# Kernel optimization log

Measured on AMD Instinct MI355X. Metric: run time of the kernel, lower is better.

The kernel has to match this reference:

```python
import jax, jax.numpy as jnp
import numpy as np

B, N, K, C, CE, H = 2, 2048, 48, 128, 128, 128
IN = 2 * C + CE  # 384
AGG_SCALE = 30.0
LN_EPS = 1e-5


def setup_inputs() -> dict:
    key = jax.random.key(0)
    ks = jax.random.split(key, 12)
    inp = {
        "node_h": jax.random.normal(ks[0], (B, N, C), jnp.float32),
        "edge_h": jax.random.normal(ks[1], (B, N, K, CE), jnp.float32),
        "edge_index": jax.random.randint(ks[2], (B, N, K), 0, N, jnp.int64),
        # message MLP: Linear(IN,H) GELU Linear(H,H) GELU Linear(H,C)
        "W1": jax.random.normal(ks[3], (IN, H), jnp.float32) / np.sqrt(IN),
        "b1": jnp.zeros((H,), jnp.float32),
        "W2": jax.random.normal(ks[4], (H, H), jnp.float32) / np.sqrt(H),
        "b2": jnp.zeros((H,), jnp.float32),
        "W3": jax.random.normal(ks[5], (H, C), jnp.float32) / np.sqrt(H),
        "b3": jnp.zeros((C,), jnp.float32),
        "Wu": jax.random.normal(ks[6], (C, C), jnp.float32) / np.sqrt(C),
        "bu": jnp.zeros((C,), jnp.float32),
        "ln_g": jnp.ones((C,), jnp.float32),
        "ln_b": jnp.zeros((C,), jnp.float32),
    }
    return inp


def _layer_norm(x, g, b):
    mu = jnp.mean(x, axis=-1, keepdims=True)
    var = jnp.var(x, axis=-1, keepdims=True)
    return (x - mu) * jax.lax.rsqrt(var + LN_EPS) * g + b


def _gelu(x):
    return jax.nn.gelu(x, approximate=False)  # torch nn.GELU default (erf)


def reference(node_h, edge_h, edge_index, W1, b1, W2, b2, W3, b3, Wu, bu, ln_g, ln_b):
    b, n, k = edge_index.shape
    c = node_h.shape[-1]
    # gather neighbor node features: (B,N,K,C)
    node_j = jnp.take_along_axis(
        node_h, edge_index.reshape(b, n * k)[..., None], axis=1
    ).reshape(b, n, k, c)
    node_i = jnp.broadcast_to(node_h[:, :, None, :], (b, n, k, c))
    edge_packed = jnp.concatenate([node_i, node_j, edge_h], axis=-1)  # (B,N,K,IN)
    # message MLP
    h = _gelu(edge_packed @ W1 + b1)
    h = _gelu(h @ W2 + b2)
    messages = (h @ W3 + b3).sum(axis=-2) / AGG_SCALE  # (B,N,C)
    # dropout is identity in eval mode
    updated_nodes = _layer_norm(node_h + messages, ln_g, ln_b)
    node_updates = updated_nodes @ Wu + bu
    out = _layer_norm(node_h + node_updates, ln_g, ln_b)
    return out
```

## Files before the change

### kernel.cpp

```cpp
#include <hip/hip_runtime.h>
#include <hip/hip_bf16.h>
#include <math.h>

#define Bn   2
#define Nn   2048
#define Kn   48
#define Cn   128
#define G2   16

typedef short bf16x8 __attribute__((ext_vector_type(8)));
typedef float f32x4  __attribute__((ext_vector_type(4)));

#if __has_builtin(__builtin_amdgcn_cvt_pk_bf16_f32)
#define HAS_PK 1
#endif

__device__ __forceinline__ short f2bf(float f) {
  union { float f; unsigned u; } v; v.f = f;
  unsigned r = v.u + 0x7fffu + ((v.u >> 16) & 1u);
  return (short)(r >> 16);
}

__device__ __forceinline__ unsigned pk2(float a, float b) {
#ifdef HAS_PK
  auto p = __builtin_amdgcn_cvt_pk_bf16_f32(a, b);
  return __builtin_bit_cast(unsigned, p);
#else
  return (unsigned)(unsigned short)f2bf(a) | ((unsigned)(unsigned short)f2bf(b) << 16);
#endif
}

__device__ __forceinline__ float gelu_f(float x) {
  float z = x * (-2.3021991f - 0.10294200f * x * x);
  float e = __builtin_amdgcn_exp2f(z);
  return x * __builtin_amdgcn_rcpf(1.0f + e);
}

__global__ void pack_weights(const float* __restrict__ W1,
                             const float* __restrict__ W2,
                             const float* __restrict__ W3,
                             const float* __restrict__ Wu,
                             short* __restrict__ ws) {
  int tid = blockIdx.x * blockDim.x + threadIdx.x;
  if (tid >= 192 * 64) return;
  int lane = tid & 63;
  int tile = tid >> 6;
  const float* W; short* dst;
  if (tile < 32)       { W = W1;         dst = ws; }
  else if (tile < 96)  { W = W1 + 16384; dst = ws + 16384; tile -= 32; }
  else if (tile < 128) { W = W2;         dst = ws + 49152; tile -= 96; }
  else if (tile < 160) { W = W3;         dst = ws + 65536; tile -= 128; }
  else                 { W = Wu;         dst = ws + 81920; tile -= 160; }
  int kt = tile >> 3, nt = tile & 7;
  int n  = nt * 16 + (lane & 15);
  int k0 = kt * 32 + (lane >> 4) * 8;
  union { short s[8]; bf16x8 v; } u8;
#pragma unroll
  for (int j = 0; j < 8; j++) u8.s[j] = f2bf(W[(k0 + j) * 128 + n]);
  *reinterpret_cast<bf16x8*>(dst + (tile << 9) + lane * 8) = u8.v;
}

__global__ __launch_bounds__(512, 8)
void node_update_kernel(const float* __restrict__ node_h,
                        const float* __restrict__ edge_h,
                        const int*   __restrict__ edge_index,
                        const short* __restrict__ wpack,
                        const float* __restrict__ b1,
                        const float* __restrict__ b2,
                        float* __restrict__ hs_out) {
  __shared__ __align__(16) char smem[25472];
  short* Xs    = (short*)smem;
  short* H1s   = (short*)smem;
  short* nhb   = (short*)(smem + 24576);
  int*   idx_s = (int*)  (smem + 25088);

  const int tid  = threadIdx.x;
  const int n0   = blockIdx.x * 2;
  const int bb   = n0 >> 11;
  const int lane = tid & 63;
  const int wave = tid >> 6;
  const int lr   = lane & 15;
  const int lq   = lane >> 4;

  const short* W1i = wpack;
  const short* W1e = wpack + 16384;
  const short* W2p = wpack + 49152;

  if (tid < 256) {
    nhb[tid] = f2bf(node_h[(size_t)n0 * Cn + tid]);
  } else if (tid < 352) {
    idx_s[tid - 256] = edge_index[n0 * Kn + (tid - 256)];
  }
  __syncthreads();

  const int gw = tid & 15;
  const int gr = tid >> 4;
#pragma unroll
  for (int k = 0; k < 3; k++) {
    int r = gr + k * 32;
    const float* src = node_h + (size_t)(bb * Nn + idx_s[r]) * Cn + gw * 8;
    float4 v0 = *reinterpret_cast<const float4*>(src);
    float4 v1 = *reinterpret_cast<const float4*>(src + 4);
    uint4 p;
    p.x = pk2(v0.x, v0.y); p.y = pk2(v0.z, v0.w);
    p.z = pk2(v1.x, v1.y); p.w = pk2(v1.z, v1.w);
    *reinterpret_cast<uint4*>(&Xs[r * 128 + ((gw ^ (r & 7)) << 3)]) = p;
  }
  __syncthreads();

  f32x4 accY[2] = {};
#pragma unroll
  for (int kt = 0; kt < 4; kt++) {
    bf16x8 avA = {}, avB = {};
    if (lr == 0) {
      avA = *reinterpret_cast<const bf16x8*>(&nhb[kt * 32 + lq * 8]);
      avB = *reinterpret_cast<const bf16x8*>(&nhb[128 + kt * 32 + lq * 8]);
    }
    bf16x8 bv = *reinterpret_cast<const bf16x8*>(W1i + ((kt * 8 + wave) << 9) + lane * 8);
    accY[0] = __builtin_amdgcn_mfma_f32_16x16x32_bf16(avA, bv, accY[0], 0, 0, 0);
    accY[1] = __builtin_amdgcn_mfma_f32_16x16x32_bf16(avB, bv, accY[1], 0, 0, 0);
  }

  f32x4 acc[6] = {};
#pragma unroll
  for (int kt = 0; kt < 4; kt++) {
    bf16x8 bf = *reinterpret_cast<const bf16x8*>(W1e + ((kt * 8 + wave) << 9) + lane * 8);
    int sw = (((kt * 4 + lq) ^ (lr & 7)) << 3);
#pragma unroll
    for (int m = 0; m < 6; m++) {
      bf16x8 a = *reinterpret_cast<const bf16x8*>(&Xs[(m * 16 + lr) * 128 + sw]);
      acc[m] = __builtin_amdgcn_mfma_f32_16x16x32_bf16(a, bf, acc[m], 0, 0, 0);
    }
  }
  __syncthreads();

#pragma unroll
  for (int k = 0; k < 3; k++) {
    int r = gr + k * 32;
    const float* src = edge_h + ((size_t)n0 * Kn + r) * Cn + gw * 8;
    float4 v0 = *reinterpret_cast<const float4*>(src);
    float4 v1 = *reinterpret_cast<const float4*>(src + 4);
    uint4 p;
    p.x = pk2(v0.x, v0.y); p.y = pk2(v0.z, v0.w);
    p.z = pk2(v1.x, v1.y); p.w = pk2(v1.z, v1.w);
    *reinterpret_cast<uint4*>(&Xs[r * 128 + ((gw ^ (r & 7)) << 3)]) = p;
  }
  __syncthreads();

#pragma unroll
  for (int kt = 4; kt < 8; kt++) {
    bf16x8 bf = *reinterpret_cast<const bf16x8*>(W1e + ((kt * 8 + wave) << 9) + lane * 8);
    int sw = ((((kt - 4) * 4 + lq) ^ (lr & 7)) << 3);
#pragma unroll
    for (int m = 0; m < 6; m++) {
      bf16x8 a = *reinterpret_cast<const bf16x8*>(&Xs[(m * 16 + lr) * 128 + sw]);
      acc[m] = __builtin_amdgcn_mfma_f32_16x16x32_bf16(a, bf, acc[m], 0, 0, 0);
    }
  }
  __syncthreads();

  {
    int col = wave * 16 + lr;
    float yiA = __shfl(accY[0][0], lr) + b1[col];
    float yiB = __shfl(accY[1][0], lr) + b1[col];
    int g = col >> 3, cl = col & 7;
#pragma unroll
    for (int mt = 0; mt < 6; mt++) {
      float yi = (mt < 3) ? yiA : yiB;
      int r0 = mt * 16 + lq * 4;
      float g0 = gelu_f(acc[mt][0] + yi);
      float g1 = gelu_f(acc[mt][1] + yi);
      float g2 = gelu_f(acc[mt][2] + yi);
      float g3 = gelu_f(acc[mt][3] + yi);
      unsigned p01 = pk2(g0, g1), p23 = pk2(g2, g3);
      H1s[(r0 + 0) * 128 + ((g ^ ((r0 + 0) & 7)) << 3) + cl] = (short)(p01 & 0xffff);
      H1s[(r0 + 1) * 128 + ((g ^ ((r0 + 1) & 7)) << 3) + cl] = (short)(p01 >> 16);
      H1s[(r0 + 2) * 128 + ((g ^ ((r0 + 2) & 7)) << 3) + cl] = (short)(p23 & 0xffff);
      H1s[(r0 + 3) * 128 + ((g ^ ((r0 + 3) & 7)) << 3) + cl] = (short)(p23 >> 16);
    }
  }
  __syncthreads();

  f32x4 acc2[6] = {};
#pragma unroll
  for (int kt = 0; kt < 4; kt++) {
    bf16x8 bf = *reinterpret_cast<const bf16x8*>(W2p + ((kt * 8 + wave) << 9) + lane * 8);
    int sw = (((kt * 4 + lq) ^ (lr & 7)) << 3);
#pragma unroll
    for (int m = 0; m < 6; m++) {
      bf16x8 a = *reinterpret_cast<const bf16x8*>(&H1s[(m * 16 + lr) * 128 + sw]);
      acc2[m] = __builtin_amdgcn_mfma_f32_16x16x32_bf16(a, bf, acc2[m], 0, 0, 0);
    }
  }
  {
    int col = wave * 16 + lr;
    float bias = b2[col];
    float sA = 0.f, sB = 0.f;
#pragma unroll
    for (int mt = 0; mt < 3; mt++)
#pragma unroll
      for (int r = 0; r < 4; r++) {
        sA += gelu_f(acc2[mt][r] + bias);
        sB += gelu_f(acc2[mt + 3][r] + bias);
      }
    sA += __shfl_xor(sA, 16);
    sA += __shfl_xor(sA, 32);
    sB += __shfl_xor(sB, 16);
    sB += __shfl_xor(sB, 32);
    if (lq == 0) {
      hs_out[(size_t)n0 * Cn + col]       = sA;
      hs_out[(size_t)(n0 + 1) * Cn + col] = sB;
    }
  }
}

__global__ __launch_bounds__(256, 4)
void tail_kernel(const float* __restrict__ node_h,
                 const short* __restrict__ wpack,
                 const float* __restrict__ b3,
                 const float* __restrict__ bu,
                 const float* __restrict__ ln_g,
                 const float* __restrict__ ln_b,
                 float* __restrict__ out) {
  __shared__ __align__(16) char sm2[24832];
  short* hsB = (short*)sm2;
  float* nhr = (float*)(sm2 + 4096);
  float* xs  = (float*)(sm2 + 12288);
  short* usB = (short*)(sm2 + 20736);

  const int tid  = threadIdx.x;
  const int lane = tid & 63;
  const int wave = tid >> 6;
  const int lr   = lane & 15;
  const int lq   = lane >> 4;
  const int n0   = blockIdx.x * G2;

  const short* W3p = wpack + 65536;
  const short* Wup = wpack + 81920;

  {
    int row = tid >> 4, seg = tid & 15;
    const float* p = node_h + (size_t)(n0 + row) * Cn + seg * 8;
    float4 a0 = *reinterpret_cast<const float4*>(p);
    float4 a1 = *reinterpret_cast<const float4*>(p + 4);
    *reinterpret_cast<float4*>(&nhr[row * 128 + seg * 8])     = a0;
    *reinterpret_cast<float4*>(&nhr[row * 128 + seg * 8 + 4]) = a1;
    const float* q = out + (size_t)(n0 + row) * Cn + seg * 8;
    float4 c0 = *reinterpret_cast<const float4*>(q);
    float4 c1 = *reinterpret_cast<const float4*>(q + 4);
    uint4 pk;
    pk.x = pk2(c0.x, c0.y); pk.y = pk2(c0.z, c0.w);
    pk.z = pk2(c1.x, c1.y); pk.w = pk2(c1.z, c1.w);
    *reinterpret_cast<uint4*>(&hsB[row * 128 + ((seg ^ (row & 7)) << 3)]) = pk;
  }
  __syncthreads();

  f32x4 am[2] = {};
#pragma unroll
  for (int kt = 0; kt < 4; kt++) {
    bf16x8 av = *reinterpret_cast<const bf16x8*>(&hsB[lr * 128 + (((kt * 4 + lq) ^ (lr & 7)) << 3)]);
    bf16x8 bv0 = *reinterpret_cast<const bf16x8*>(W3p + ((kt * 8 + wave * 2 + 0) << 9) + lane * 8);
    bf16x8 bv1 = *reinterpret_cast<const bf16x8*>(W3p + ((kt * 8 + wave * 2 + 1) << 9) + lane * 8);
    am[0] = __builtin_amdgcn_mfma_f32_16x16x32_bf16(av, bv0, am[0], 0, 0, 0);
    am[1] = __builtin_amdgcn_mfma_f32_16x16x32_bf16(av, bv1, am[1], 0, 0, 0);
  }
#pragma unroll
  for (int j = 0; j < 2; j++) {
    int col = (wave * 2 + j) * 16 + lr;
    float bb = 48.0f * b3[col];
#pragma unroll
    for (int r = 0; r < 4; r++) {
      int row = lq * 4 + r;
      xs[row * 132 + col] = nhr[row * 128 + col] + (am[j][r] + bb) * (1.0f / 30.0f);
    }
  }
  __syncthreads();

  const float lg1 = ln_g[lane],      lb1v = ln_b[lane];
  const float lg2 = ln_g[lane + 64], lb2v = ln_b[lane + 64];
#pragma unroll
  for (int s = 0; s < 4; s++) {
    int row = wave * 4 + s;
    float v1 = xs[row * 132 + lane];
    float v2 = xs[row * 132 + lane + 64];
    float s1 = v1 + v2, s2 = v1 * v1 + v2 * v2;
#pragma unroll
    for (int off = 32; off >= 1; off >>= 1) {
      s1 += __shfl_xor(s1, off);
      s2 += __shfl_xor(s2, off);
    }
    float mu = s1 * (1.f / 128.f);
    float var = s2 * (1.f / 128.f) - mu * mu;
    float rstd = rsqrtf(var + 1e-5f);
    unsigned u12 = pk2((v1 - mu) * rstd * lg1 + lb1v,
                       (v2 - mu) * rstd * lg2 + lb2v);
    int sw = (row & 7);
    usB[row * 128 + (((lane >> 3) ^ sw) << 3) + (lane & 7)]       = (short)(u12 & 0xffff);
    usB[row * 128 + ((((lane >> 3) + 8) ^ sw) << 3) + (lane & 7)] = (short)(u12 >> 16);
  }
  __syncthreads();

  f32x4 au[2] = {};
#pragma unroll
  for (int kt = 0; kt < 4; kt++) {
    bf16x8 av = *reinterpret_cast<const bf16x8*>(&usB[lr * 128 + (((kt * 4 + lq) ^ (lr & 7)) << 3)]);
    bf16x8 bv0 = *reinterpret_cast<const bf16x8*>(Wup + ((kt * 8 + wave * 2 + 0) << 9) + lane * 8);
    bf16x8 bv1 = *reinterpret_cast<const bf16x8*>(Wup + ((kt * 8 + wave * 2 + 1) << 9) + lane * 8);
    au[0] = __builtin_amdgcn_mfma_f32_16x16x32_bf16(av, bv0, au[0], 0, 0, 0);
    au[1] = __builtin_amdgcn_mfma_f32_16x16x32_bf16(av, bv1, au[1], 0, 0, 0);
  }
  __syncthreads();
#pragma unroll
  for (int j = 0; j < 2; j++) {
    int col = (wave * 2 + j) * 16 + lr;
    float bb = bu[col];
#pragma unroll
    for (int r = 0; r < 4; r++) {
      int row = lq * 4 + r;
      xs[row * 132 + col] = nhr[row * 128 + col] + au[j][r] + bb;
    }
  }
  __syncthreads();

#pragma unroll
  for (int s = 0; s < 4; s++) {
    int row = wave * 4 + s;
    float v1 = xs[row * 132 + lane];
    float v2 = xs[row * 132 + lane + 64];
    float s1 = v1 + v2, s2 = v1 * v1 + v2 * v2;
#pragma unroll
    for (int off = 32; off >= 1; off >>= 1) {
      s1 += __shfl_xor(s1, off);
      s2 += __shfl_xor(s2, off);
    }
    float mu = s1 * (1.f / 128.f);
    float var = s2 * (1.f / 128.f) - mu * mu;
    float rstd = rsqrtf(var + 1e-5f);
    out[(size_t)(n0 + row) * Cn + lane]      = (v1 - mu) * rstd * lg1 + lb1v;
    out[(size_t)(n0 + row) * Cn + lane + 64] = (v2 - mu) * rstd * lg2 + lb2v;
  }
}

extern "C" void kernel_launch(void* const* d_in, const int* in_sizes, int n_in,
                              void* d_out, int out_size, void* d_ws, size_t ws_size,
                              hipStream_t stream) {
  const float* node_h     = (const float*)d_in[0];
  const float* edge_h     = (const float*)d_in[1];
  const int*   edge_index = (const int*)  d_in[2];
  const float* W1 = (const float*)d_in[3];
  const float* b1 = (const float*)d_in[4];
  const float* W2 = (const float*)d_in[5];
  const float* b2 = (const float*)d_in[6];
  const float* W3 = (const float*)d_in[7];
  const float* b3 = (const float*)d_in[8];
  const float* Wu = (const float*)d_in[9];
  const float* bu = (const float*)d_in[10];
  const float* ln_g = (const float*)d_in[11];
  const float* ln_b = (const float*)d_in[12];
  float* out   = (float*)d_out;
  short* wpack = (short*)d_ws;

  pack_weights<<<48, 256, 0, stream>>>(W1, W2, W3, Wu, wpack);
  node_update_kernel<<<(Bn * Nn) / 2, 512, 0, stream>>>(
      node_h, edge_h, edge_index, wpack, b1, b2, out);
  tail_kernel<<<(Bn * Nn) / G2, 256, 0, stream>>>(
      node_h, wpack, b3, bu, ln_g, ln_b, out);
}
```

Baseline: 209.0 us.

## Prefetch gathered rows, edge features and weights into registers to overlap loads

The node_update kernel now issues the global loads for neighbour rows, weight fragments, biases and edge_h into registers early. Those loads run while earlier MFMA work (the node_i projection and the first half of the layer-1 GEMM) executes, and the bf16 pack and LDS store happen later. This is meant to hide global memory latency behind compute instead of stalling at each gather-then-sync step. The extra live registers force the launch-bounds occupancy hint down from 8 to 6, which may reduce latency hiding across waves.

```diff
diff --git a/kernel.cpp b/kernel.cpp
--- a/kernel.cpp
+++ b/kernel.cpp
@@ -60,7 +60,7 @@
   *reinterpret_cast<bf16x8*>(dst + (tile << 9) + lane * 8) = u8.v;
 }
 
-__global__ __launch_bounds__(512, 8)
+__global__ __launch_bounds__(512, 6)
 void node_update_kernel(const float* __restrict__ node_h,
                         const float* __restrict__ edge_h,
                         const int*   __restrict__ edge_index,
@@ -86,6 +86,14 @@
   const short* W1e = wpack + 16384;
   const short* W2p = wpack + 49152;
 
+  bf16x8 w1i[4];
+#pragma unroll
+  for (int kt = 0; kt < 4; kt++)
+    w1i[kt] = *reinterpret_cast<const bf16x8*>(W1i + ((kt * 8 + wave) << 9) + lane * 8);
+  const int colw = wave * 16 + lr;
+  const float b1v = b1[colw];
+  const float b2v = b2[colw];
+
   if (tid < 256) {
     nhb[tid] = f2bf(node_h[(size_t)n0 * Cn + tid]);
   } else if (tid < 352) {
@@ -95,18 +103,15 @@
 
   const int gw = tid & 15;
   const int gr = tid >> 4;
+
+  float4 na[3], nb[3];
 #pragma unroll
   for (int k = 0; k < 3; k++) {
     int r = gr + k * 32;
     const float* src = node_h + (size_t)(bb * Nn + idx_s[r]) * Cn + gw * 8;
-    float4 v0 = *reinterpret_cast<const float4*>(src);
-    float4 v1 = *reinterpret_cast<const float4*>(src + 4);
-    uint4 p;
-    p.x = pk2(v0.x, v0.y); p.y = pk2(v0.z, v0.w);
-    p.z = pk2(v1.x, v1.y); p.w = pk2(v1.z, v1.w);
-    *reinterpret_cast<uint4*>(&Xs[r * 128 + ((gw ^ (r & 7)) << 3)]) = p;
-  }
-  __syncthreads();
+    na[k] = *reinterpret_cast<const float4*>(src);
+    nb[k] = *reinterpret_cast<const float4*>(src + 4);
+  }
 
   f32x4 accY[2] = {};
 #pragma unroll
@@ -116,15 +121,60 @@
       avA = *reinterpret_cast<const bf16x8*>(&nhb[kt * 32 + lq * 8]);
       avB = *reinterpret_cast<const bf16x8*>(&nhb[128 + kt * 32 + lq * 8]);
     }
-    bf16x8 bv = *reinterpret_cast<const bf16x8*>(W1i + ((kt * 8 + wave) << 9) + lane * 8);
-    accY[0] = __builtin_amdgcn_mfma_f32_16x16x32_bf16(avA, bv, accY[0], 0, 0, 0);
-    accY[1] = __builtin_amdgcn_mfma_f32_16x16x32_bf16(avB, bv, accY[1], 0, 0, 0);
+    accY[0] = __builtin_amdgcn_mfma_f32_16x16x32_bf16(avA, w1i[kt], accY[0], 0, 0, 0);
+    accY[1] = __builtin_amdgcn_mfma_f32_16x16x32_bf16(avB, w1i[kt], accY[1], 0, 0, 0);
+  }
+  const float yiA = __shfl(accY[0][0], lr) + b1v;
+  const float yiB = __shfl(accY[1][0], lr) + b1v;
+
+#pragma unroll
+  for (int k = 0; k < 3; k++) {
+    int r = gr + k * 32;
+    uint4 p;
+    p.x = pk2(na[k].x, na[k].y); p.y = pk2(na[k].z, na[k].w);
+    p.z = pk2(nb[k].x, nb[k].y); p.w = pk2(nb[k].z, nb[k].w);
+    *reinterpret_cast<uint4*>(&Xs[r * 128 + ((gw ^ (r & 7)) << 3)]) = p;
+  }
+  __syncthreads();
+
+  bf16x8 w1a[4];
+#pragma unroll
+  for (int kt = 0; kt < 4; kt++)
+    w1a[kt] = *reinterpret_cast<const bf16x8*>(W1e + ((kt * 8 + wave) << 9) + lane * 8);
+  float4 ea[3], eb[3];
+#pragma unroll
+  for (int k = 0; k < 3; k++) {
+    int r = gr + k * 32;
+    const float* src = edge_h + ((size_t)n0 * Kn + r) * Cn + gw * 8;
+    ea[k] = *reinterpret_cast<const float4*>(src);
+    eb[k] = *reinterpret_cast<const float4*>(src + 4);
   }
 
   f32x4 acc[6] = {};
 #pragma unroll
   for (int kt = 0; kt < 4; kt++) {
-    bf16x8 bf = *reinterpret_cast<const bf16x8*>(W1e + ((kt * 8 + wave) << 9) + lane * 8);
+    int sw = (((kt * 4 + lq) ^ (lr & 7)) << 3);
+#pragma unroll
+    for (int m = 0; m < 6; m++) {
+      bf16x8 a = *reinterpret_cast<const bf16x8*>(&Xs[(m * 16 + lr) * 128 + sw]);
+      acc[m] = __builtin_amdgcn_mfma_f32_16x16x32_bf16(a, w1a[kt], acc[m], 0, 0, 0);
+    }
+  }
+  __syncthreads();
+
+#pragma unroll
+  for (int k = 0; k < 3; k++) {
+    int r = gr + k * 32;
+    uint4 p;
+    p.x = pk2(ea[k].x, ea[k].y); p.y = pk2(ea[k].z, ea[k].w);
+    p.z = pk2(eb[k].x, eb[k].y); p.w = pk2(eb[k].z, eb[k].w);
+    *reinterpret_cast<uint4*>(&Xs[r * 128 + ((gw ^ (r & 7)) << 3)]) = p;
+  }
+  __syncthreads();
+
+#pragma unroll
+  for (int kt = 0; kt < 4; kt++) {
+    bf16x8 bf = *reinterpret_cast<const bf16x8*>(W1e + (((kt + 4) * 8 + wave) << 9) + lane * 8);
     int sw = (((kt * 4 + lq) ^ (lr & 7)) << 3);
 #pragma unroll
     for (int m = 0; m < 6; m++) {
@@ -134,36 +184,8 @@
   }
   __syncthreads();
 
-#pragma unroll
-  for (int k = 0; k < 3; k++) {
-    int r = gr + k * 32;
-    const float* src = edge_h + ((size_t)n0 * Kn + r) * Cn + gw * 8;
-    float4 v0 = *reinterpret_cast<const float4*>(src);
-    float4 v1 = *reinterpret_cast<const float4*>(src + 4);
-    uint4 p;
-    p.x = pk2(v0.x, v0.y); p.y = pk2(v0.z, v0.w);
-    p.z = pk2(v1.x, v1.y); p.w = pk2(v1.z, v1.w);
-    *reinterpret_cast<uint4*>(&Xs[r * 128 + ((gw ^ (r & 7)) << 3)]) = p;
-  }
-  __syncthreads();
-
-#pragma unroll
-  for (int kt = 4; kt < 8; kt++) {
-    bf16x8 bf = *reinterpret_cast<const bf16x8*>(W1e + ((kt * 8 + wave) << 9) + lane * 8);
-    int sw = ((((kt - 4) * 4 + lq) ^ (lr & 7)) << 3);
-#pragma unroll
-    for (int m = 0; m < 6; m++) {
-      bf16x8 a = *reinterpret_cast<const bf16x8*>(&Xs[(m * 16 + lr) * 128 + sw]);
-      acc[m] = __builtin_amdgcn_mfma_f32_16x16x32_bf16(a, bf, acc[m], 0, 0, 0);
-    }
-  }
-  __syncthreads();
-
   {
-    int col = wave * 16 + lr;
-    float yiA = __shfl(accY[0][0], lr) + b1[col];
-    float yiB = __shfl(accY[1][0], lr) + b1[col];
-    int g = col >> 3, cl = col & 7;
+    int g = colw >> 3, cl = colw & 7;
 #pragma unroll
     for (int mt = 0; mt < 6; mt++) {
       float yi = (mt < 3) ? yiA : yiB;
@@ -193,23 +215,21 @@
     }
   }
   {
-    int col = wave * 16 + lr;
-    float bias = b2[col];
     float sA = 0.f, sB = 0.f;
 #pragma unroll
     for (int mt = 0; mt < 3; mt++)
 #pragma unroll
       for (int r = 0; r < 4; r++) {
-        sA += gelu_f(acc2[mt][r] + bias);
-        sB += gelu_f(acc2[mt + 3][r] + bias);
+        sA += gelu_f(acc2[mt][r] + b2v);
+        sB += gelu_f(acc2[mt + 3][r] + b2v);
       }
     sA += __shfl_xor(sA, 16);
     sA += __shfl_xor(sA, 32);
     sB += __shfl_xor(sB, 16);
     sB += __shfl_xor(sB, 32);
     if (lq == 0) {
-      hs_out[(size_t)n0 * Cn + col]       = sA;
-      hs_out[(size_t)(n0 + 1) * Cn + col] = sB;
+      hs_out[(size_t)n0 * Cn + colw]       = sA;
+      hs_out[(size_t)(n0 + 1) * Cn + colw] = sB;
     }
   }
 }
```

After: 202.7 us. 1.03x faster.
